# Performance work log

Measured on AMD Instinct MI355X. Metric: run time of the kernel, lower is better.

Reference implementation:

```python
import jax, jax.numpy as jnp
import numpy as np

# Graph layout: B equal-sized graphs, contiguous node ids.
B, NG, EG = 64, 2000, 64000          # graphs, nodes/graph, edges/graph
K = 1600                              # ceil(0.8 * NG) — TopKPooling ratio=0.8
N, E = B * NG, B * EG
FEAT_DIM, EMB, G1, G2, DENSE, NCLS = 10000, 64, 32, 32, 64, 10


def setup_inputs() -> dict:
    key = jax.random.key(0)
    ks = jax.random.split(key, 12)
    x = jax.random.randint(ks[0], (N, 1), 0, FEAT_DIM)
    # random edges within each graph, then offset by graph base node id
    e = jax.random.randint(ks[1], (2, B, EG), 0, NG) + (jnp.arange(B) * NG)[None, :, None]
    edge_index = e.reshape(2, E)
    batch = jnp.repeat(jnp.arange(B), NG)
    sc = 0.05
    return {
        "x": x, "edge_index": edge_index, "batch": batch,
        "emb": jax.random.normal(ks[2], (FEAT_DIM, EMB), jnp.float32) * sc,
        "W1": jax.random.normal(ks[3], (EMB, G1), jnp.float32) * sc,
        "b1": jnp.zeros((G1,), jnp.float32),
        "W2": jax.random.normal(ks[4], (G1, G2), jnp.float32) * sc,
        "b2": jnp.zeros((G2,), jnp.float32),
        "pool_w": jax.random.normal(ks[5], (G2,), jnp.float32) * sc,
        "dense_W": jax.random.normal(ks[6], (G2, DENSE), jnp.float32) * sc,
        "dense_b": jnp.zeros((DENSE,), jnp.float32),
        "out_W": jax.random.normal(ks[7], (DENSE, NCLS), jnp.float32) * sc,
        "out_b": jnp.zeros((NCLS,), jnp.float32),
    }


def gcn_layer(h, src, dst, W, b):
    """PyG GCNConv: add self-loops, symmetric D^-1/2 A D^-1/2 aggregation."""
    n = h.shape[0]
    loop = jnp.arange(n)
    s = jnp.concatenate([src, loop])
    d = jnp.concatenate([dst, loop])
    h = h @ W                                                   # [N, out]
    deg = jax.ops.segment_sum(jnp.ones_like(d, dtype=h.dtype), d, num_segments=n)
    dinv = jnp.where(deg > 0, deg ** -0.5, 0.0)
    norm = dinv[s] * dinv[d]                                    # [E+N]
    out = jax.ops.segment_sum(h[s] * norm[:, None], d, num_segments=n)
    return out + b


def reference(x, edge_index, batch, emb, W1, b1, W2, b2, pool_w,
              dense_W, dense_b, out_W, out_b):
    h = emb[x[:, 0]]                                            # [N, EMB]
    src, dst = edge_index[0], edge_index[1]
    h = jax.nn.relu(gcn_layer(h, src, dst, W1, b1))
    h = jax.nn.relu(gcn_layer(h, src, dst, W2, b2))
    # TopKPooling: score = tanh(x.w / ||w||); keep top ceil(0.8*NG) per graph,
    # scale kept features by their scores. Equal graph sizes -> static shapes.
    score = jnp.tanh(h @ pool_w / jnp.linalg.norm(pool_w))      # [N]
    sb = score.reshape(B, NG)
    hb = h.reshape(B, NG, G2)
    vals, idx = jax.lax.top_k(sb, K)                            # [B, K]
    hp = jnp.take_along_axis(hb, idx[:, :, None], axis=1) * vals[:, :, None]
    g = hp.max(axis=1)                                          # global max pool [B, G2]
    d = jax.nn.relu(g @ dense_W + dense_b)
    return d @ out_W + out_b                                    # [B, NCLS]
```

## Files before the change

### kernel.cpp

```cpp
#include <hip/hip_runtime.h>
#include <hip/hip_fp16.h>
#include <math.h>

#define NB 64
#define NGRAPH 2000
#define EGRAPH 64000
#define NN (NB*NGRAPH)
#define NE (NB*EGRAPH)
#define KSEL 1600
#define FEAT 10000
#define EMBD 64
#define G1D 32
#define G2D 32
#define DENSED 64
#define NCLSD 10
#define NCHUNK 8
#define CHUNK_E (EGRAPH/NCHUNK)
#define AGG_PARTS 4
#define NPP (NGRAPH/AGG_PARTS)


__device__ __forceinline__ float4 ld_row8h(const char* base, unsigned byteoff)
{
    uint2 u = *(const uint2*)(base + byteoff);
    __half2 p0 = *(__half2*)&u.x;
    __half2 p1 = *(__half2*)&u.y;
    float2 f0 = __half22float2(p0);
    float2 f1 = __half22float2(p1);
    return make_float4(f0.x, f0.y, f1.x, f1.y);
}

__device__ __forceinline__ void st_row8h(__half* dst, float4 v)
{
    __half2 p0 = __floats2half2_rn(v.x, v.y);
    __half2 p1 = __floats2half2_rn(v.z, v.w);
    uint2 u;
    u.x = *(unsigned*)&p0;
    u.y = *(unsigned*)&p1;
    *(uint2*)dst = u;
}

__device__ __forceinline__ void acc8h(const char* base, unsigned off,
                                      __half2& lo, __half2& hi)
{
    uint2 u = *(const uint2*)(base + off);
    lo = __hadd2(lo, *(__half2*)&u.x);
    hi = __hadd2(hi, *(__half2*)&u.y);
}

__device__ __forceinline__ float4 h2tof4(__half2 lo, __half2 hi)
{
    float2 a = __half22float2(lo);
    float2 b = __half22float2(hi);
    return make_float4(a.x, a.y, b.x, b.y);
}

__device__ __forceinline__ __half2 shfl_xor_h2(__half2 v, int off)
{
    int i = *(int*)&v;
    i = __shfl_xor(i, off, 32);
    return *(__half2*)&i;
}

__global__ __launch_bounds__(256) void prep_kernel(const int* __restrict__ ei,
                                                   int* __restrict__ chist,
                                                   const float* __restrict__ emb,
                                                   const float* __restrict__ W1,
                                                   float* __restrict__ embW)
{
    __shared__ float shmem[2048];
    const int tid = threadIdx.x;
    if (blockIdx.x < 512) {
        int* hist = (int*)shmem;
        const int lb = blockIdx.x;
        const int xcd = lb & 7, t = lb >> 3;
        const int g = xcd * 8 + (t >> 3);
        const int q = t & 7;
        const int base_e = g * EGRAPH + q * CHUNK_E;
        const int base_n = g * NGRAPH;
        for (int v = tid; v < NGRAPH; v += 256) hist[v] = 0;
        __syncthreads();
        for (int k = tid; k < CHUNK_E; k += 256) {
            int d = ei[NE + base_e + k];
            atomicAdd(&hist[d - base_n], 1);
        }
        __syncthreads();
        int* out = chist + (size_t)(g * NCHUNK + q) * NGRAPH;
        for (int v = tid; v < NGRAPH; v += 256) out[v] = hist[v];
    } else {
        float* W1s = shmem;
        for (int i = tid; i < EMBD * G1D; i += 256) W1s[i] = W1[i];
        __syncthreads();
        int id = (blockIdx.x - 512) * 256 + tid;
        int r = id >> 5, c = id & 31;
        if (r >= FEAT) return;
        const float* er = emb + r * EMBD;
        float acc = 0.f;
        #pragma unroll 8
        for (int k = 0; k < EMBD; ++k) acc += er[k] * W1s[k * G1D + c];
        embW[r * G1D + c] = acc;
    }
}

__global__ __launch_bounds__(256) void scan_graph(int* __restrict__ chist,
                                                  float* __restrict__ dinv,
                                                  int* __restrict__ row_start)
{
    __shared__ int hist[NGRAPH];
    __shared__ int csA[256];
    __shared__ int csB[256];
    const int b = (blockIdx.x & 7) * 8 + (blockIdx.x >> 3);
    const int tid = threadIdx.x;
    const int base_n = b * NGRAPH, base_e = b * EGRAPH;
    int* ch = chist + (size_t)b * NCHUNK * NGRAPH;

    for (int v = tid; v < NGRAPH; v += 256) {
        int tot = 0;
        #pragma unroll
        for (int q = 0; q < NCHUNK; ++q) tot += ch[q * NGRAPH + v];
        hist[v] = tot;
        dinv[base_n + v] = rsqrtf((float)(tot + 1));
    }
    __syncthreads();
    if (tid < 250) {
        int s = 0;
        #pragma unroll
        for (int i = 0; i < 8; ++i) s += hist[tid * 8 + i];
        csA[tid] = s;
    }
    __syncthreads();
    int* sb = csA; int* db = csB;
    for (int off = 1; off < 256; off <<= 1) {
        int v = 0;
        if (tid < 250) { v = sb[tid]; if (tid >= off) v += sb[tid - off]; }
        if (tid < 250) db[tid] = v;
        __syncthreads();
        int* t = sb; sb = db; db = t;
    }
    if (tid < 250) {
        int run = (tid == 0) ? 0 : sb[tid - 1];
        #pragma unroll
        for (int i = 0; i < 8; ++i) {
            int idx = tid * 8 + i;
            int c = hist[idx];
            row_start[base_n + idx] = base_e + run;
            hist[idx] = base_e + run;
            run += c;
        }
    }
    __syncthreads();
    for (int v = tid; v < NGRAPH; v += 256) {
        int run = hist[v];
        #pragma unroll
        for (int q = 0; q < NCHUNK; ++q) {
            int c = ch[q * NGRAPH + v];
            ch[q * NGRAPH + v] = run;
            run += c;
        }
    }
}

__global__ __launch_bounds__(1024) void mid_kernel(const int* __restrict__ ei,
                                                   const int* __restrict__ cbase,
                                                   int* __restrict__ csr)
{
    __shared__ int cur[NGRAPH];
    const int tid = threadIdx.x;
    const int lb = blockIdx.x;
    const int xcd = lb & 7, t = lb >> 3;
    const int g = xcd * 8 + (t >> 3);
    const int q = t & 7;
    const int base_n = g * NGRAPH;
    const int* cb = cbase + (size_t)(g * NCHUNK + q) * NGRAPH;
    for (int v = tid; v < NGRAPH; v += 1024) cur[v] = cb[v];
    __syncthreads();
    const int base_e4 = (g * EGRAPH + q * CHUNK_E) >> 2;
    const int4* srcp = (const int4*)ei + base_e4;
    const int4* dstp = (const int4*)(ei + NE) + base_e4;
    for (int k = tid; k < CHUNK_E / 4; k += 1024) {
        int4 d4 = dstp[k];
        int4 s4 = srcp[k];
        int pos, sl;
        pos = atomicAdd(&cur[d4.x - base_n], 1);
        sl = s4.x - base_n; csr[pos] = (sl << 6) + (sl << 3);
        pos = atomicAdd(&cur[d4.y - base_n], 1);
        sl = s4.y - base_n; csr[pos] = (sl << 6) + (sl << 3);
        pos = atomicAdd(&cur[d4.z - base_n], 1);
        sl = s4.z - base_n; csr[pos] = (sl << 6) + (sl << 3);
        pos = atomicAdd(&cur[d4.w - base_n], 1);
        sl = s4.w - base_n; csr[pos] = (sl << 6) + (sl << 3);
    }
}


__global__ __launch_bounds__(1024) void agg1_kernel(const int* __restrict__ x,
                                                    const float* __restrict__ embW,
                                                    const float* __restrict__ dinv,
                                                    const int* __restrict__ row_start,
                                                    const int* __restrict__ csr,
                                                    const float* __restrict__ b1,
                                                    const float* __restrict__ W2,
                                                    __half* __restrict__ Bout)
{
    __shared__ uint2 table2[NGRAPH * 9];
    __shared__ __align__(16) __half2 hshh[32][16];
    const int lb = blockIdx.x;
    const int xcd = lb & 7, t = lb >> 3;
    const int b = xcd * 8 + (t >> 2);
    const int part = t & 3;
    const int tid = threadIdx.x;
    const int base_n = b * NGRAPH;

    {
        for (int i = tid; i < NGRAPH * 8; i += 1024) {
            int v = i >> 3, r = i & 7;
            int xv = x[base_n + v];
            float dv = dinv[base_n + v];
            float4 e = ((const float4*)(embW + (size_t)xv * G1D))[r];
            __half2 p0 = __floats2half2_rn(e.x * dv, e.y * dv);
            __half2 p1 = __floats2half2_rn(e.z * dv, e.w * dv);
            uint2 u;
            u.x = *(unsigned*)&p0;
            u.y = *(unsigned*)&p1;
            table2[v * 9 + r] = u;
        }
    }
    __syncthreads();

    const char* Lbase = (const char*)table2;
    const int hw = tid >> 5;
    const int hl = tid & 31;
    const int slot = hl >> 3;
    const int r = hl & 7;
    const int roff = r << 3;
    const float4 bias4 = ((const float4*)b1)[r];

    __half2 w2c2[G1D / 2];
    #pragma unroll
    for (int k = 0; k < G1D / 2; ++k)
        w2c2[k] = __floats2half2_rn(W2[(2 * k) * G2D + hl],
                                    (2 * k + 1 < G1D) ? W2[(2 * k + 1) * G2D + hl] : 0.f);

    const __half2 z2 = __float2half2_rn(0.f);

    const int vloc0 = part * NPP + hw * 16;
    const int vend = part * NPP + NPP;
    int v = base_n + vloc0;
    int rs = row_start[v];
    int re = (v == NN - 1) ? NE : row_start[v + 1];
    int s0 = csr[rs + slot];
    int s1 = csr[rs + slot + 4];
    int s2 = csr[rs + slot + 8];
    int s3 = csr[rs + slot + 12];

    for (int i = 0; i < 16; ++i) {
        int vloc = vloc0 + i;
        if (vloc >= vend) break;
        int re_next = (v + 1 >= NN - 1) ? NE : row_start[v + 2];
        int n0 = csr[re + slot];
        int n1 = csr[re + slot + 4];
        int n2 = csr[re + slot + 8];
        int n3 = csr[re + slot + 12];

        int me = rs + ((re - rs) & ~15);
        __half2 l0 = z2, h0 = z2, l1 = z2, h1 = z2;
        __half2 l2 = z2, h2 = z2, l3 = z2, h3 = z2;
        if (slot == 0)
            acc8h(Lbase, (unsigned)((vloc << 6) + (vloc << 3) + roff), l0, h0);
        int j = rs + slot;
        while (j < me) {
            int jn = j + 16;
            int t0 = csr[jn];
            int t1 = csr[jn + 4];
            int t2 = csr[jn + 8];
            int t3 = csr[jn + 12];
            acc8h(Lbase, (unsigned)(s0 + roff), l0, h0);
            acc8h(Lbase, (unsigned)(s1 + roff), l1, h1);
            acc8h(Lbase, (unsigned)(s2 + roff), l2, h2);
            acc8h(Lbase, (unsigned)(s3 + roff), l3, h3);
            j = jn; s0 = t0; s1 = t1; s2 = t2; s3 = t3;
        }
        {
            int jt = me + slot;
            if (jt < re)      acc8h(Lbase, (unsigned)(s0 + roff), l0, h0);
            if (jt + 4 < re)  acc8h(Lbase, (unsigned)(s1 + roff), l1, h1);
            if (jt + 8 < re)  acc8h(Lbase, (unsigned)(s2 + roff), l2, h2);
            if (jt + 12 < re) acc8h(Lbase, (unsigned)(s3 + roff), l3, h3);
        }
        __half2 L = __hadd2(__hadd2(l0, l1), __hadd2(l2, l3));
        __half2 H = __hadd2(__hadd2(h0, h1), __hadd2(h2, h3));
        L = __hadd2(L, shfl_xor_h2(L, 8));
        H = __hadd2(H, shfl_xor_h2(H, 8));
        L = __hadd2(L, shfl_xor_h2(L, 16));
        H = __hadd2(H, shfl_xor_h2(H, 16));
        float4 accf = h2tof4(L, H);
        float dv = dinv[v];
        if (slot == 0) {
            float4 h4;
            h4.x = fmaxf(dv * accf.x + bias4.x, 0.f);
            h4.y = fmaxf(dv * accf.y + bias4.y, 0.f);
            h4.z = fmaxf(dv * accf.z + bias4.z, 0.f);
            h4.w = fmaxf(dv * accf.w + bias4.w, 0.f);
            __half2 p0 = __floats2half2_rn(h4.x, h4.y);
            __half2 p1 = __floats2half2_rn(h4.z, h4.w);
            uint2 u;
            u.x = *(unsigned*)&p0;
            u.y = *(unsigned*)&p1;
            ((uint2*)&hshh[hw][0])[r] = u;
        }
        __half2 o2a = z2, o2b = z2;
        const uint4* hrow4 = (const uint4*)&hshh[hw][0];
        #pragma unroll
        for (int q = 0; q < 4; ++q) {
            uint4 u = hrow4[q];
            o2a = __hfma2(*(__half2*)&u.x, w2c2[4 * q + 0], o2a);
            o2b = __hfma2(*(__half2*)&u.y, w2c2[4 * q + 1], o2b);
            o2a = __hfma2(*(__half2*)&u.z, w2c2[4 * q + 2], o2a);
            o2b = __hfma2(*(__half2*)&u.w, w2c2[4 * q + 3], o2b);
        }
        __half2 os = __hadd2(o2a, o2b);
        float2 of = __half22float2(os);
        Bout[(size_t)v * G2D + hl] = __float2half(dv * (of.x + of.y));
        v = v + 1;
        rs = re; re = re_next; s0 = n0; s1 = n1; s2 = n2; s3 = n3;
    }
}

__global__ __launch_bounds__(1024) void agg2_kernel(const __half* __restrict__ Bin,
                                                    const float* __restrict__ dinv,
                                                    const int* __restrict__ row_start,
                                                    const int* __restrict__ csr,
                                                    const float* __restrict__ b2,
                                                    const float* __restrict__ pool_w,
                                                    __half* __restrict__ h2out,
                                                    float* __restrict__ scores)
{
    __shared__ uint2 table2[NGRAPH * 9];
    const int lb = blockIdx.x;
    const int xcd = lb & 7, t = lb >> 3;
    const int b = xcd * 8 + (t >> 2);
    const int part = t & 3;
    const int tid = threadIdx.x;
    const int base_n = b * NGRAPH;

    {
        const uint2* src = (const uint2*)(Bin + (size_t)base_n * G1D);
        for (int i = tid; i < NGRAPH * 8; i += 1024)
            table2[(i >> 3) * 9 + (i & 7)] = src[i];
    }
    __syncthreads();

    const char* Lbase = (const char*)table2;
    const int hw = tid >> 5;
    const int hl = tid & 31;
    const int slot = hl >> 3;
    const int r = hl & 7;
    const int roff = r << 3;
    const float4 bias4 = ((const float4*)b2)[r];
    const float4 pw4 = ((const float4*)pool_w)[r];

    float pw = pool_w[hl];
    float nsq = pw * pw;
    #pragma unroll
    for (int off = 16; off; off >>= 1) nsq += __shfl_xor(nsq, off, 32);
    const float inv_norm = rsqrtf(nsq);

    const __half2 z2 = __float2half2_rn(0.f);

    const int vloc0 = part * NPP + hw * 16;
    const int vend = part * NPP + NPP;
    int v = base_n + vloc0;
    int rs = row_start[v];
    int re = (v == NN - 1) ? NE : row_start[v + 1];
    int s0 = csr[rs + slot];
    int s1 = csr[rs + slot + 4];
    int s2 = csr[rs + slot + 8];
    int s3 = csr[rs + slot + 12];

    for (int i = 0; i < 16; ++i) {
        int vloc = vloc0 + i;
        if (vloc >= vend) break;
        int re_next = (v + 1 >= NN - 1) ? NE : row_start[v + 2];
        int n0 = csr[re + slot];
        int n1 = csr[re + slot + 4];
        int n2 = csr[re + slot + 8];
        int n3 = csr[re + slot + 12];

        int me = rs + ((re - rs) & ~15);
        __half2 l0 = z2, h0 = z2, l1 = z2, h1 = z2;
        __half2 l2 = z2, h2 = z2, l3 = z2, h3 = z2;
        if (slot == 0)
            acc8h(Lbase, (unsigned)((vloc << 6) + (vloc << 3) + roff), l0, h0);
        int j = rs + slot;
        while (j < me) {
            int jn = j + 16;
            int t0 = csr[jn];
            int t1 = csr[jn + 4];
            int t2 = csr[jn + 8];
            int t3 = csr[jn + 12];
            acc8h(Lbase, (unsigned)(s0 + roff), l0, h0);
            acc8h(Lbase, (unsigned)(s1 + roff), l1, h1);
            acc8h(Lbase, (unsigned)(s2 + roff), l2, h2);
            acc8h(Lbase, (unsigned)(s3 + roff), l3, h3);
            j = jn; s0 = t0; s1 = t1; s2 = t2; s3 = t3;
        }
        {
            int jt = me + slot;
            if (jt < re)      acc8h(Lbase, (unsigned)(s0 + roff), l0, h0);
            if (jt + 4 < re)  acc8h(Lbase, (unsigned)(s1 + roff), l1, h1);
            if (jt + 8 < re)  acc8h(Lbase, (unsigned)(s2 + roff), l2, h2);
            if (jt + 12 < re) acc8h(Lbase, (unsigned)(s3 + roff), l3, h3);
        }
        __half2 L = __hadd2(__hadd2(l0, l1), __hadd2(l2, l3));
        __half2 H = __hadd2(__hadd2(h0, h1), __hadd2(h2, h3));
        L = __hadd2(L, shfl_xor_h2(L, 8));
        H = __hadd2(H, shfl_xor_h2(H, 8));
        L = __hadd2(L, shfl_xor_h2(L, 16));
        H = __hadd2(H, shfl_xor_h2(H, 16));
        float4 accf = h2tof4(L, H);
        float dv = dinv[v];
        float4 h4;
        h4.x = fmaxf(dv * accf.x + bias4.x, 0.f);
        h4.y = fmaxf(dv * accf.y + bias4.y, 0.f);
        h4.z = fmaxf(dv * accf.z + bias4.z, 0.f);
        h4.w = fmaxf(dv * accf.w + bias4.w, 0.f);
        if (slot == 0)
            st_row8h(h2out + (size_t)v * G2D + r * 4, h4);
        float tt = h4.x * pw4.x + h4.y * pw4.y + h4.z * pw4.z + h4.w * pw4.w;
        tt += __shfl_xor(tt, 1, 32);
        tt += __shfl_xor(tt, 2, 32);
        tt += __shfl_xor(tt, 4, 32);
        if (hl == 0) scores[v] = tanhf(tt * inv_norm);
        v = v + 1;
        rs = re; re = re_next; s0 = n0; s1 = n1; s2 = n2; s3 = n3;
    }
}

__global__ __launch_bounds__(1024) void topk_pool_mlp(const __half* __restrict__ h2,
                                                      const float* __restrict__ scores,
                                                      const float* __restrict__ dense_W,
                                                      const float* __restrict__ dense_b,
                                                      const float* __restrict__ out_W,
                                                      const float* __restrict__ out_b,
                                                      float* __restrict__ out)
{
    __shared__ unsigned keys[NGRAPH];
    __shared__ float    sval[NGRAPH];
    __shared__ unsigned char inc[NGRAPH];
    __shared__ int  hist[256];
    __shared__ int  csA[256];
    __shared__ int  csB[256];
    __shared__ int  sel[2];
    __shared__ int  redc[16];
    __shared__ float redf[128][32];
    __shared__ float redp[8][32];
    __shared__ float gvec[32];
    __shared__ float dvec[DENSED];
    const int b = (blockIdx.x & 7) * 8 + (blockIdx.x >> 3);
    const int tid = threadIdx.x;
    const int base_n = b * NGRAPH;

    for (int v = tid; v < NGRAPH; v += 1024) {
        float f = scores[base_n + v];
        sval[v] = f;
        unsigned u = __float_as_uint(f);
        keys[v] = (u & 0x80000000u) ? ~u : (u | 0x80000000u);
    }
    __syncthreads();

    unsigned T = 0;
    int need = KSEL;
    #pragma unroll
    for (int pass = 0; pass < 4; ++pass) {
        const int s = 24 - pass * 8;
        const unsigned hi_mask = (pass == 0) ? 0u : (0xFFFFFFFFu << (s + 8));
        if (tid < 256) hist[tid] = 0;
        __syncthreads();
        for (int v = tid; v < NGRAPH; v += 1024) {
            unsigned k = keys[v];
            if ((k & hi_mask) == (T & hi_mask))
                atomicAdd(&hist[(k >> s) & 255], 1);
        }
        __syncthreads();
        if (tid < 256) csA[tid] = hist[255 - tid];
        __syncthreads();
        int* sb = csA; int* db = csB;
        for (int off = 1; off < 256; off <<= 1) {
            int val = 0;
            if (tid < 256) {
                val = sb[tid];
                if (tid >= off) val += sb[tid - off];
                db[tid] = val;
            }
            __syncthreads();
            int* t = sb; sb = db; db = t;
        }
        if (tid < 256) {
            const int d = tid;
            int suf_d = sb[255 - d];
            int suf_d1 = (d == 255) ? 0 : sb[254 - d];
            if (suf_d >= need && suf_d1 < need) {
                sel[0] = d;
                sel[1] = suf_d1;
            }
        }
        __syncthreads();
        T |= ((unsigned)sel[0]) << s;
        need -= sel[1];
        __syncthreads();
    }

    const int wid = tid >> 6, ln = tid & 63;
    int cg = 0, ce = 0;
    for (int v = tid; v < NGRAPH; v += 1024) {
        cg += (keys[v] > T) ? 1 : 0;
        ce += (keys[v] == T) ? 1 : 0;
    }
    int packed = (cg << 16) | ce;
    #pragma unroll
    for (int off = 32; off; off >>= 1) packed += __shfl_down(packed, off, 64);
    if (ln == 0) redc[wid] = packed;
    __syncthreads();
    int tot = 0;
    #pragma unroll
    for (int w = 0; w < 16; ++w) tot += redc[w];
    int m_gt = tot >> 16, m_eq = tot & 0xffff;
    int needed = KSEL - m_gt;
    float fT = (T & 0x80000000u) ? __uint_as_float(T & 0x7fffffffu)
                                 : __uint_as_float(~T);
    if (m_eq == needed || fT == 0.0f) {
        for (int v = tid; v < NGRAPH; v += 1024) inc[v] = (keys[v] >= T) ? 1 : 0;
    } else {
        if (tid == 0) {
            int take = 0;
            for (int v = 0; v < NGRAPH; ++v) {
                unsigned k = keys[v];
                if (k > T) inc[v] = 1;
                else if (k == T && take < needed) { inc[v] = 1; ++take; }
                else inc[v] = 0;
            }
        }
    }
    __syncthreads();

    {
        const int rowslot = tid >> 3;
        const int c4 = tid & 7;
        float4 m4 = make_float4(-INFINITY, -INFINITY, -INFINITY, -INFINITY);
        const char* h2base = (const char*)h2;
        for (int v = rowslot; v < NGRAPH; v += 128) {
            float4 hrow = ld_row8h(h2base,
                                   (unsigned)((base_n + v) * (G2D * 2) + c4 * 8));
            float sv = inc[v] ? sval[v] : 0.f;
            float big = inc[v] ? 0.f : -INFINITY;
            m4.x = fmaxf(m4.x, sv * hrow.x + big);
            m4.y = fmaxf(m4.y, sv * hrow.y + big);
            m4.z = fmaxf(m4.z, sv * hrow.z + big);
            m4.w = fmaxf(m4.w, sv * hrow.w + big);
        }
        redf[rowslot][c4 * 4 + 0] = m4.x;
        redf[rowslot][c4 * 4 + 1] = m4.y;
        redf[rowslot][c4 * 4 + 2] = m4.z;
        redf[rowslot][c4 * 4 + 3] = m4.w;
    }
    __syncthreads();
    if (tid < 256) {
        const int col = tid & 31, part = tid >> 5;
        float g = redf[part * 16][col];
        #pragma unroll
        for (int rr = 1; rr < 16; ++rr) g = fmaxf(g, redf[part * 16 + rr][col]);
        redp[part][col] = g;
    }
    __syncthreads();
    if (tid < 32) {
        float g = redp[0][tid];
        #pragma unroll
        for (int p = 1; p < 8; ++p) g = fmaxf(g, redp[p][tid]);
        gvec[tid] = g;
    }
    __syncthreads();
    if (tid < DENSED) {
        float t = dense_b[tid];
        #pragma unroll
        for (int k = 0; k < G2D; ++k) t += gvec[k] * dense_W[k * DENSED + tid];
        dvec[tid] = fmaxf(t, 0.f);
    }
    __syncthreads();
    if (tid < NCLSD) {
        float o = out_b[tid];
        #pragma unroll
        for (int j = 0; j < DENSED; ++j) o += dvec[j] * out_W[j * NCLSD + tid];
        out[b * NCLSD + tid] = o;
    }
}

extern "C" void kernel_launch(void* const* d_in, const int* in_sizes, int n_in,
                              void* d_out, int out_size, void* d_ws, size_t ws_size,
                              hipStream_t stream)
{
    (void)in_sizes; (void)n_in; (void)out_size; (void)ws_size;
    const int*   x       = (const int*)  d_in[0];
    const int*   edge    = (const int*)  d_in[1];
    const float* emb     = (const float*)d_in[3];
    const float* W1      = (const float*)d_in[4];
    const float* b1      = (const float*)d_in[5];
    const float* W2      = (const float*)d_in[6];
    const float* b2      = (const float*)d_in[7];
    const float* pool_w  = (const float*)d_in[8];
    const float* dense_W = (const float*)d_in[9];
    const float* dense_b = (const float*)d_in[10];
    const float* out_W   = (const float*)d_in[11];
    const float* out_b   = (const float*)d_in[12];
    float* outp = (float*)d_out;

    char* ws = (char*)d_ws;
    float*  embW      = (float*)ws;
    __half* H2h       = (__half*)(ws + 1280000);
    __half* Bh        = (__half*)(ws + 1280000 + 8192000);
    float*  dinv      = (float*)(ws + 1280000 + 2*8192000);
    int*    row_start = (int*)((char*)dinv + (size_t)NN*4);
    int*    csr       = (int*)((char*)row_start + (size_t)NN*4);
    float*  scores    = (float*)((char*)csr + (size_t)(NE+16)*4);

    int* chist = (int*)Bh;

    prep_kernel<<<512 + (FEAT * G1D) / 256, 256, 0, stream>>>(edge, chist, emb, W1, embW);
    scan_graph<<<NB, 256, 0, stream>>>(chist, dinv, row_start);
    mid_kernel<<<512, 1024, 0, stream>>>(edge, chist, csr);
    agg1_kernel<<<NB * AGG_PARTS, 1024, 0, stream>>>(x, embW, dinv, row_start, csr, b1, W2, Bh);
    agg2_kernel<<<NB * AGG_PARTS, 1024, 0, stream>>>(Bh, dinv, row_start, csr, b2, pool_w, H2h, scores);
    topk_pool_mlp<<<NB, 1024, 0, stream>>>(H2h, scores, dense_W, dense_b, out_W, out_b, outp);
}
```

Measured before the change: 220.5 us.

## Fuse top-k pooling and MLP into agg2 via last-block-done counter

Removes the separate topk_pool_mlp launch. Each graph's four agg2 blocks increment a per-graph atomic counter after a threadfence, and the last block to finish runs the radix top-k, pooling and MLP using the reused shared table as scratch. The counter is reset in scan_graph. This saves one kernel launch and its gap, but the tail work now runs on only 64 blocks at the end of agg2 and relies on the fence for visibility of the other blocks' h2 and score writes.

```diff
diff --git a/kernel.cpp b/kernel.cpp
--- a/kernel.cpp
+++ b/kernel.cpp
@@ -104,7 +104,8 @@
 
 __global__ __launch_bounds__(256) void scan_graph(int* __restrict__ chist,
                                                   float* __restrict__ dinv,
-                                                  int* __restrict__ row_start)
+                                                  int* __restrict__ row_start,
+                                                  int* __restrict__ gcount)
 {
     __shared__ int hist[NGRAPH];
     __shared__ int csA[256];
@@ -113,6 +114,8 @@
     const int tid = threadIdx.x;
     const int base_n = b * NGRAPH, base_e = b * EGRAPH;
     int* ch = chist + (size_t)b * NCHUNK * NGRAPH;
+
+    if (tid == 0) gcount[b] = 0;
 
     for (int v = tid; v < NGRAPH; v += 256) {
         int tot = 0;
@@ -239,7 +242,7 @@
     #pragma unroll
     for (int k = 0; k < G1D / 2; ++k)
         w2c2[k] = __floats2half2_rn(W2[(2 * k) * G2D + hl],
-                                    (2 * k + 1 < G1D) ? W2[(2 * k + 1) * G2D + hl] : 0.f);
+                                    W2[(2 * k + 1) * G2D + hl]);
 
     const __half2 z2 = __float2half2_rn(0.f);
 
@@ -333,9 +336,16 @@
                                                     const float* __restrict__ b2,
                                                     const float* __restrict__ pool_w,
                                                     __half* __restrict__ h2out,
-                                                    float* __restrict__ scores)
+                                                    float* __restrict__ scores,
+                                                    const float* __restrict__ dense_W,
+                                                    const float* __restrict__ dense_b,
+                                                    const float* __restrict__ out_W,
+                                                    const float* __restrict__ out_b,
+                                                    float* __restrict__ out,
+                                                    int* __restrict__ gcount)
 {
     __shared__ uint2 table2[NGRAPH * 9];
+    __shared__ int lastflag;
     const int lb = blockIdx.x;
     const int xcd = lb & 7, t = lb >> 3;
     const int b = xcd * 8 + (t >> 2);
@@ -434,37 +444,33 @@
         v = v + 1;
         rs = re; re = re_next; s0 = n0; s1 = n1; s2 = n2; s3 = n3;
     }
-}
-
-__global__ __launch_bounds__(1024) void topk_pool_mlp(const __half* __restrict__ h2,
-                                                      const float* __restrict__ scores,
-                                                      const float* __restrict__ dense_W,
-                                                      const float* __restrict__ dense_b,
-                                                      const float* __restrict__ out_W,
-                                                      const float* __restrict__ out_b,
-                                                      float* __restrict__ out)
-{
-    __shared__ unsigned keys[NGRAPH];
-    __shared__ float    sval[NGRAPH];
-    __shared__ unsigned char inc[NGRAPH];
-    __shared__ int  hist[256];
-    __shared__ int  csA[256];
-    __shared__ int  csB[256];
-    __shared__ int  sel[2];
-    __shared__ int  redc[16];
-    __shared__ float redf[128][32];
-    __shared__ float redp[8][32];
-    __shared__ float gvec[32];
-    __shared__ float dvec[DENSED];
-    const int b = (blockIdx.x & 7) * 8 + (blockIdx.x >> 3);
-    const int tid = threadIdx.x;
-    const int base_n = b * NGRAPH;
-
-    for (int v = tid; v < NGRAPH; v += 1024) {
-        float f = scores[base_n + v];
-        sval[v] = f;
+
+    __threadfence();
+    __syncthreads();
+    if (tid == 0) lastflag = atomicAdd(&gcount[b], 1);
+    __syncthreads();
+    if (lastflag != AGG_PARTS - 1) return;
+
+    char* sm = (char*)table2;
+    unsigned* keys = (unsigned*)sm;
+    float* sval    = (float*)(sm + 8000);
+    unsigned char* incb = (unsigned char*)(sm + 16000);
+    int* hist      = (int*)(sm + 18000);
+    int* csA       = (int*)(sm + 19024);
+    int* csB       = (int*)(sm + 20048);
+    int* sel2      = (int*)(sm + 21072);
+    int* redc      = (int*)(sm + 21088);
+    float (*redf)[32] = (float(*)[32])(sm + 21152);
+    float (*redp)[32] = (float(*)[32])(sm + 37536);
+    float* gvec    = (float*)(sm + 38560);
+    float* dvec    = (float*)(sm + 38688);
+    __syncthreads();
+
+    for (int vv = tid; vv < NGRAPH; vv += 1024) {
+        float f = scores[base_n + vv];
+        sval[vv] = f;
         unsigned u = __float_as_uint(f);
-        keys[v] = (u & 0x80000000u) ? ~u : (u | 0x80000000u);
+        keys[vv] = (u & 0x80000000u) ? ~u : (u | 0x80000000u);
     }
     __syncthreads();
 
@@ -476,8 +482,8 @@
         const unsigned hi_mask = (pass == 0) ? 0u : (0xFFFFFFFFu << (s + 8));
         if (tid < 256) hist[tid] = 0;
         __syncthreads();
-        for (int v = tid; v < NGRAPH; v += 1024) {
-            unsigned k = keys[v];
+        for (int vv = tid; vv < NGRAPH; vv += 1024) {
+            unsigned k = keys[vv];
             if ((k & hi_mask) == (T & hi_mask))
                 atomicAdd(&hist[(k >> s) & 255], 1);
         }
@@ -493,28 +499,28 @@
                 db[tid] = val;
             }
             __syncthreads();
-            int* t = sb; sb = db; db = t;
+            int* tt2 = sb; sb = db; db = tt2;
         }
         if (tid < 256) {
             const int d = tid;
             int suf_d = sb[255 - d];
             int suf_d1 = (d == 255) ? 0 : sb[254 - d];
             if (suf_d >= need && suf_d1 < need) {
-                sel[0] = d;
-                sel[1] = suf_d1;
+                sel2[0] = d;
+                sel2[1] = suf_d1;
             }
         }
         __syncthreads();
-        T |= ((unsigned)sel[0]) << s;
-        need -= sel[1];
+        T |= ((unsigned)sel2[0]) << s;
+        need -= sel2[1];
         __syncthreads();
     }
 
     const int wid = tid >> 6, ln = tid & 63;
     int cg = 0, ce = 0;
-    for (int v = tid; v < NGRAPH; v += 1024) {
-        cg += (keys[v] > T) ? 1 : 0;
-        ce += (keys[v] == T) ? 1 : 0;
+    for (int vv = tid; vv < NGRAPH; vv += 1024) {
+        cg += (keys[vv] > T) ? 1 : 0;
+        ce += (keys[vv] == T) ? 1 : 0;
     }
     int packed = (cg << 16) | ce;
     #pragma unroll
@@ -529,15 +535,15 @@
     float fT = (T & 0x80000000u) ? __uint_as_float(T & 0x7fffffffu)
                                  : __uint_as_float(~T);
     if (m_eq == needed || fT == 0.0f) {
-        for (int v = tid; v < NGRAPH; v += 1024) inc[v] = (keys[v] >= T) ? 1 : 0;
+        for (int vv = tid; vv < NGRAPH; vv += 1024) incb[vv] = (keys[vv] >= T) ? 1 : 0;
     } else {
         if (tid == 0) {
             int take = 0;
-            for (int v = 0; v < NGRAPH; ++v) {
-                unsigned k = keys[v];
-                if (k > T) inc[v] = 1;
-                else if (k == T && take < needed) { inc[v] = 1; ++take; }
-                else inc[v] = 0;
+            for (int vv = 0; vv < NGRAPH; ++vv) {
+                unsigned k = keys[vv];
+                if (k > T) incb[vv] = 1;
+                else if (k == T && take < needed) { incb[vv] = 1; ++take; }
+                else incb[vv] = 0;
             }
         }
     }
@@ -547,12 +553,12 @@
         const int rowslot = tid >> 3;
         const int c4 = tid & 7;
         float4 m4 = make_float4(-INFINITY, -INFINITY, -INFINITY, -INFINITY);
-        const char* h2base = (const char*)h2;
-        for (int v = rowslot; v < NGRAPH; v += 128) {
+        const char* h2base = (const char*)h2out;
+        for (int vv = rowslot; vv < NGRAPH; vv += 128) {
             float4 hrow = ld_row8h(h2base,
-                                   (unsigned)((base_n + v) * (G2D * 2) + c4 * 8));
-            float sv = inc[v] ? sval[v] : 0.f;
-            float big = inc[v] ? 0.f : -INFINITY;
+                                   (unsigned)((base_n + vv) * (G2D * 2) + c4 * 8));
+            float sv = incb[vv] ? sval[vv] : 0.f;
+            float big = incb[vv] ? 0.f : -INFINITY;
             m4.x = fmaxf(m4.x, sv * hrow.x + big);
             m4.y = fmaxf(m4.y, sv * hrow.y + big);
             m4.z = fmaxf(m4.z, sv * hrow.z + big);
@@ -565,11 +571,11 @@
     }
     __syncthreads();
     if (tid < 256) {
-        const int col = tid & 31, part = tid >> 5;
-        float g = redf[part * 16][col];
-        #pragma unroll
-        for (int rr = 1; rr < 16; ++rr) g = fmaxf(g, redf[part * 16 + rr][col]);
-        redp[part][col] = g;
+        const int col = tid & 31, pp = tid >> 5;
+        float g = redf[pp * 16][col];
+        #pragma unroll
+        for (int rr = 1; rr < 16; ++rr) g = fmaxf(g, redf[pp * 16 + rr][col]);
+        redp[pp][col] = g;
     }
     __syncthreads();
     if (tid < 32) {
@@ -580,16 +586,16 @@
     }
     __syncthreads();
     if (tid < DENSED) {
-        float t = dense_b[tid];
-        #pragma unroll
-        for (int k = 0; k < G2D; ++k) t += gvec[k] * dense_W[k * DENSED + tid];
-        dvec[tid] = fmaxf(t, 0.f);
+        float tacc = dense_b[tid];
+        #pragma unroll
+        for (int k = 0; k < G2D; ++k) tacc += gvec[k] * dense_W[k * DENSED + tid];
+        dvec[tid] = fmaxf(tacc, 0.f);
     }
     __syncthreads();
     if (tid < NCLSD) {
         float o = out_b[tid];
         #pragma unroll
-        for (int j = 0; j < DENSED; ++j) o += dvec[j] * out_W[j * NCLSD + tid];
+        for (int jj = 0; jj < DENSED; ++jj) o += dvec[jj] * out_W[jj * NCLSD + tid];
         out[b * NCLSD + tid] = o;
     }
 }
@@ -621,13 +627,15 @@
     int*    row_start = (int*)((char*)dinv + (size_t)NN*4);
     int*    csr       = (int*)((char*)row_start + (size_t)NN*4);
     float*  scores    = (float*)((char*)csr + (size_t)(NE+16)*4);
+    int*    gcount    = (int*)(scores + NN);
 
     int* chist = (int*)Bh;
 
     prep_kernel<<<512 + (FEAT * G1D) / 256, 256, 0, stream>>>(edge, chist, emb, W1, embW);
-    scan_graph<<<NB, 256, 0, stream>>>(chist, dinv, row_start);
+    scan_graph<<<NB, 256, 0, stream>>>(chist, dinv, row_start, gcount);
     mid_kernel<<<512, 1024, 0, stream>>>(edge, chist, csr);
     agg1_kernel<<<NB * AGG_PARTS, 1024, 0, stream>>>(x, embW, dinv, row_start, csr, b1, W2, Bh);
-    agg2_kernel<<<NB * AGG_PARTS, 1024, 0, stream>>>(Bh, dinv, row_start, csr, b2, pool_w, H2h, scores);
-    topk_pool_mlp<<<NB, 1024, 0, stream>>>(H2h, scores, dense_W, dense_b, out_W, out_b, outp);
-}
+    agg2_kernel<<<NB * AGG_PARTS, 1024, 0, stream>>>(Bh, dinv, row_start, csr, b2, pool_w,
+                                                     H2h, scores, dense_W, dense_b,
+                                                     out_W, out_b, outp, gcount);
+}
```

Measured after the change: 296.5 us. 34.5% more time.
